# Optimization experiments

Measured on AMD Instinct MI355X. Metric: run time of the kernel, lower is better.

## Reference

```python
import jax, jax.numpy as jnp
import numpy as np

# Module config (init_kwargs)
K_PERIODS = 5
PMAX = 512
MIN_PERIOD_THRESHOLD = 2

B, T, N = 32, 2048, 128


def setup_inputs() -> dict:
    key = jax.random.key(0)
    x = jax.random.normal(key, (B, T, N), dtype=jnp.float32)
    return {"x": x}


def reference(x):
    """Faithful dense/padded JAX version of PeriodicityTransform.forward (mask=None).

    The torch module emits ragged PeriodGroups keyed by (cycles, period).
    Since jit requires static shapes, we return the same per-(series, freq)
    information in padded form:
      tiles   : [BN, K, T]  flattened folded tile (row-major cycle x period),
                 zero-padded past take = cycles*periods
      periods : [BN, K] int32
      cycles  : [BN, K] int32
    tiles[bn,k,:take].reshape(cycles, period) equals the torch tile exactly.
    """
    Bq, Tq, Nq = x.shape
    BN = Bq * Nq
    seqs = jnp.transpose(x, (0, 2, 1)).reshape(BN, Tq)  # [BN, T]

    # --- _topk_freq ---
    spec = jnp.fft.rfft(seqs, axis=-1)                   # [BN, T//2+1]
    mag2 = spec.real ** 2 + spec.imag ** 2
    mag2 = mag2.at[..., 0].set(0.0)                      # kill DC
    k = min(K_PERIODS, mag2.shape[-1] - 1)
    _, kidx = jax.lax.top_k(mag2, k)                     # [BN, K]
    kidx = jnp.maximum(kidx, 1).astype(jnp.int32)

    # --- period / cycle computation (valid_lengths == T, no mask) ---
    lengths = jnp.int32(Tq)
    periods = lengths // kidx                            # [BN, K]
    periods = jnp.minimum(periods, PMAX)
    min_period = min(MIN_PERIOD_THRESHOLD, Tq)
    periods = jnp.maximum(periods, min_period)
    periods = jnp.maximum(periods, 1)
    cycles = jnp.maximum(lengths // periods, 1)          # [BN, K]

    take = cycles * periods                              # [BN, K], <= T
    t = jnp.arange(Tq, dtype=jnp.int32)                  # [T]
    start = Tq - take                                    # [BN, K]
    gather_idx = jnp.clip(start[..., None] + t, 0, Tq - 1)  # [BN, K, T]
    valid = t[None, None, :] < take[..., None]           # [BN, K, T]

    src = jnp.broadcast_to(seqs[:, None, :], (BN, k, Tq))
    tiles = jnp.take_along_axis(src, gather_idx, axis=-1)
    tiles = jnp.where(valid, tiles, jnp.zeros((), dtype=tiles.dtype))
    return tiles, periods, cycles
```

## Files before the change

### kernel.cpp

```cpp
#include <hip/hip_runtime.h>

#define B_ 32
#define T_ 2048
#define N_ 128
#define K_ 5
#define BN_ (B_ * N_)
#define PMAX_ 512
#define MINP_ 2

static constexpr double PI_D = 3.14159265358979323846264338327950288;
static constexpr double S2_D = 0.70710678118654752440084436210485;

typedef float nfloat4 __attribute__((ext_vector_type(4)));

struct cd { double r, i; };

__device__ __forceinline__ void bf_w(cd& u, cd& v, double wr, double wi) {
    const double tr = v.r * wr - v.i * wi;
    const double ti = v.r * wi + v.i * wr;
    v.r = u.r - tr; v.i = u.i - ti;
    u.r += tr;      u.i += ti;
}
__device__ __forceinline__ void bf_1(cd& u, cd& v) {
    const double tr = v.r, ti = v.i;
    v.r = u.r - tr; v.i = u.i - ti;
    u.r += tr;      u.i += ti;
}
__device__ __forceinline__ void bf_mi(cd& u, cd& v) {
    const double tr = v.i, ti = -v.r;
    v.r = u.r - tr; v.i = u.i - ti;
    u.r += tr;      u.i += ti;
}
__device__ __forceinline__ int sw(int i) { return i ^ ((i >> 5) & 31); }

__global__ __launch_bounds__(256) void pt_twiddle(double2* __restrict__ tw) {
    const int m = blockIdx.x * 256 + threadIdx.x;
    if (m < 1024) {
        double s, c;
        sincos(-2.0 * PI_D * (double)m / 2048.0, &s, &c);
        tw[m] = make_double2(c, s);
    }
}

__global__ __launch_bounds__(256, 3) void pt_fft_tiles(const float* __restrict__ x,
                                                       float* __restrict__ out,
                                                       const double2* __restrict__ tw) {
    __shared__ double re[2048];
    __shared__ double im[2048];
    __shared__ __align__(16) float seqA[2052];
    __shared__ __align__(16) float seqB[2052];
    __shared__ double wredv[4];
    __shared__ int    wredi[4];
    __shared__ int sh_per[2][K_], sh_cyc[2][K_], sh_take[2][K_];

    const int i0  = blockIdx.x;
    const int q   = ((i0 & 7) << 8) | (i0 >> 3);
    const int bn0 = q * 2;
    const int b   = bn0 >> 7;
    const int n   = bn0 & 127;
    const int tid = threadIdx.x;

    const float* xp = x + (size_t)b * T_ * N_ + n;
#pragma unroll
    for (int m = 0; m < 8; ++m) {
        const int t = tid + 256 * m;
        const float2 v = *(const float2*)(xp + (size_t)t * N_);
        seqA[t] = v.x;
        seqB[t] = v.y;
        const int p = sw((int)(__brev((unsigned)t) >> 21));
        re[p] = (double)v.x;
        im[p] = (double)v.y;
    }
    __syncthreads();

    {
        const int base = tid * 8;
        cd E[8];
#pragma unroll
        for (int j = 0; j < 8; ++j) { const int p = sw(base + j); E[j].r = re[p]; E[j].i = im[p]; }
        bf_1(E[0], E[1]); bf_1(E[2], E[3]); bf_1(E[4], E[5]); bf_1(E[6], E[7]);
        bf_1(E[0], E[2]); bf_mi(E[1], E[3]); bf_1(E[4], E[6]); bf_mi(E[5], E[7]);
        bf_1(E[0], E[4]); bf_w(E[1], E[5], S2_D, -S2_D);
        bf_mi(E[2], E[6]); bf_w(E[3], E[7], -S2_D, -S2_D);
#pragma unroll
        for (int j = 0; j < 8; ++j) { const int p = sw(base + j); re[p] = E[j].r; im[p] = E[j].i; }
    }
    __syncthreads();

#pragma unroll
    for (int r = 0; r < 2; ++r) {
        const int s    = 4 + 3 * r;
        const int h    = 1 << (s - 1);
        const int bq   = tid & (h - 1);
        const int g    = tid >> (s - 1);
        const int base = g * 8 * h + bq;
        const double2 w1  = tw[bq << (11 - s)];
        const double2 w2a = tw[bq << (10 - s)];
        const double2 w2b = tw[(bq + h) << (10 - s)];
        const double2 w30 = tw[bq << (9 - s)];
        const double2 w31 = tw[(bq + h) << (9 - s)];
        const double2 w32 = tw[(bq + 2 * h) << (9 - s)];
        const double2 w33 = tw[(bq + 3 * h) << (9 - s)];
        cd E[8];
#pragma unroll
        for (int j = 0; j < 8; ++j) { const int p = sw(base + j * h); E[j].r = re[p]; E[j].i = im[p]; }
        bf_w(E[0], E[1], w1.x, w1.y);   bf_w(E[2], E[3], w1.x, w1.y);
        bf_w(E[4], E[5], w1.x, w1.y);   bf_w(E[6], E[7], w1.x, w1.y);
        bf_w(E[0], E[2], w2a.x, w2a.y); bf_w(E[1], E[3], w2b.x, w2b.y);
        bf_w(E[4], E[6], w2a.x, w2a.y); bf_w(E[5], E[7], w2b.x, w2b.y);
        bf_w(E[0], E[4], w30.x, w30.y); bf_w(E[1], E[5], w31.x, w31.y);
        bf_w(E[2], E[6], w32.x, w32.y); bf_w(E[3], E[7], w33.x, w33.y);
#pragma unroll
        for (int j = 0; j < 8; ++j) { const int p = sw(base + j * h); re[p] = E[j].r; im[p] = E[j].i; }
        __syncthreads();
    }

#pragma unroll
    for (int u = 0; u < 2; ++u) {
        const int bb = tid + 256 * u;
        const double2 wA = tw[bb << 1];
        const double2 wB = tw[bb];
        const double2 wC = tw[bb + 512];
        const int p0 = sw(bb), p1 = sw(bb + 512), p2 = sw(bb + 1024), p3 = sw(bb + 1536);
        cd E0 = {re[p0], im[p0]}, E1 = {re[p1], im[p1]};
        cd E2 = {re[p2], im[p2]}, E3 = {re[p3], im[p3]};
        bf_w(E0, E1, wA.x, wA.y); bf_w(E2, E3, wA.x, wA.y);
        bf_w(E0, E2, wB.x, wB.y); bf_w(E1, E3, wC.x, wC.y);
        re[p0] = E0.r; im[p0] = E0.i; re[p1] = E1.r; im[p1] = E1.i;
        re[p2] = E2.r; im[p2] = E2.i; re[p3] = E3.r; im[p3] = E3.i;
    }
    __syncthreads();

    double magsA[4], magsB[4];
#pragma unroll
    for (int m = 0; m < 4; ++m) {
        const int k  = 1 + tid + 256 * m;
        const int nk = 2048 - k;
        const int pk = sw(k), pn = sw(nk);
        const double zr = re[pk], zi = im[pk];
        const double yr = re[pn], yi = im[pn];
        const double ar = zr + yr, ai = zi - yi;
        const double br = zi + yi, bi = yr - zr;
        magsA[m] = ar * ar + ai * ai;
        magsB[m] = br * br + bi * bi;
    }
    __syncthreads();
#pragma unroll
    for (int m = 0; m < 4; ++m) {
        const int pk = sw(1 + tid + 256 * m);
        re[pk] = magsA[m];
        im[pk] = magsB[m];
    }
    __syncthreads();

    const int half = tid >> 7;
    const int lt   = tid & 127;
    const int wid  = tid >> 6;
    double* marr = half ? im : re;
    for (int it = 0; it < K_; ++it) {
        double bestv = -2.0;
        int    besti = 1 << 30;
#pragma unroll
        for (int m = 0; m < 8; ++m) {
            const int k = 1 + lt + 128 * m;
            const double v = marr[sw(k)];
            if (v > bestv || (v == bestv && k < besti)) { bestv = v; besti = k; }
        }
#pragma unroll
        for (int off = 32; off > 0; off >>= 1) {
            const double v2 = __shfl_down(bestv, off);
            const int    i2 = __shfl_down(besti, off);
            if (v2 > bestv || (v2 == bestv && i2 < besti)) { bestv = v2; besti = i2; }
        }
        if ((tid & 63) == 0) { wredv[wid] = bestv; wredi[wid] = besti; }
        __syncthreads();
        if (lt == 0) {
            double vb = wredv[2 * half]; int ib = wredi[2 * half];
            const double v1 = wredv[2 * half + 1]; const int i1 = wredi[2 * half + 1];
            if (v1 > vb || (v1 == vb && i1 < ib)) { vb = v1; ib = i1; }
            marr[sw(ib)] = -1.0;
            int period = T_ / ib;
            if (period > PMAX_) period = PMAX_;
            if (period < MINP_) period = MINP_;
            const int cyc = T_ / period;
            sh_per[half][it]  = period;
            sh_cyc[half][it]  = cyc;
            sh_take[half][it] = period * cyc;
        }
        __syncthreads();
    }

    const size_t TILES = (size_t)BN_ * K_ * T_;
    if (tid < 2 * K_) {
        const int s2 = tid / K_, k2 = tid % K_;
        out[TILES + (size_t)(bn0 + s2) * K_ + k2]                      = (float)sh_per[s2][k2];
        out[TILES + (size_t)BN_ * K_ + (size_t)(bn0 + s2) * K_ + k2]   = (float)sh_cyc[s2][k2];
    }

    float* rowA = out + (size_t)bn0 * (K_ * T_);
#pragma unroll
    for (int m = 0; m < 20; ++m) {
        const int e  = tid + 256 * m;
        const int s2 = (e >= K_ * (T_ / 4)) ? 1 : 0;
        const int w  = e - s2 * (K_ * (T_ / 4));
        const int k  = w >> 9;
        const int p4 = (w & 511) << 2;
        const int take  = sh_take[s2][k];
        const int start = T_ - take;
        const float4* sq4 = (const float4*)(s2 ? seqB : seqA);
        const int idx = start + p4;
        int a0 = idx >> 2;
        if (a0 > 511) a0 = 511;
        const int sh = idx & 3;
        const float4 lo = sq4[a0];
        const float4 hi = sq4[a0 + 1];
        float r0, r1, r2, r3;
        if (sh == 0)      { r0 = lo.x; r1 = lo.y; r2 = lo.z; r3 = lo.w; }
        else if (sh == 1) { r0 = lo.y; r1 = lo.z; r2 = lo.w; r3 = hi.x; }
        else if (sh == 2) { r0 = lo.z; r1 = lo.w; r2 = hi.x; r3 = hi.y; }
        else              { r0 = lo.w; r1 = hi.x; r2 = hi.y; r3 = hi.z; }
        nfloat4 v;
        v.x = (p4 + 0 < take) ? r0 : 0.0f;
        v.y = (p4 + 1 < take) ? r1 : 0.0f;
        v.z = (p4 + 2 < take) ? r2 : 0.0f;
        v.w = (p4 + 3 < take) ? r3 : 0.0f;
        __builtin_nontemporal_store(v, (nfloat4*)(rowA + (size_t)(s2 * K_ + k) * T_ + p4));
    }
}

extern "C" void kernel_launch(void* const* d_in, const int* in_sizes, int n_in,
                              void* d_out, int out_size, void* d_ws, size_t ws_size,
                              hipStream_t stream) {
    const float* x = (const float*)d_in[0];
    float* out = (float*)d_out;
    double2* tw = (double2*)d_ws;

    pt_twiddle<<<dim3(4), dim3(256), 0, stream>>>(tw);
    pt_fft_tiles<<<dim3(BN_ / 2), dim3(256), 0, stream>>>(x, out, tw);
}
```

Baseline: 245.2 us.

## Scatter tiles from register-held inputs instead of staging sequences in LDS

```diff
diff --git a/kernel.cpp b/kernel.cpp
--- a/kernel.cpp
+++ b/kernel.cpp
@@ -11,8 +11,6 @@
 static constexpr double PI_D = 3.14159265358979323846264338327950288;
 static constexpr double S2_D = 0.70710678118654752440084436210485;
 
-typedef float nfloat4 __attribute__((ext_vector_type(4)));
-
 struct cd { double r, i; };
 
 __device__ __forceinline__ void bf_w(cd& u, cd& v, double wr, double wi) {
@@ -42,16 +40,14 @@
     }
 }
 
-__global__ __launch_bounds__(256, 3) void pt_fft_tiles(const float* __restrict__ x,
+__global__ __launch_bounds__(256, 4) void pt_fft_tiles(const float* __restrict__ x,
                                                        float* __restrict__ out,
                                                        const double2* __restrict__ tw) {
     __shared__ double re[2048];
     __shared__ double im[2048];
-    __shared__ __align__(16) float seqA[2052];
-    __shared__ __align__(16) float seqB[2052];
     __shared__ double wredv[4];
     __shared__ int    wredi[4];
-    __shared__ int sh_per[2][K_], sh_cyc[2][K_], sh_take[2][K_];
+    __shared__ int sh_take[2][K_];
 
     const int i0  = blockIdx.x;
     const int q   = ((i0 & 7) << 8) | (i0 >> 3);
@@ -61,15 +57,17 @@
     const int tid = threadIdx.x;
 
     const float* xp = x + (size_t)b * T_ * N_ + n;
+    float2 v[8];
+#pragma unroll
+    for (int m = 0; m < 8; ++m)
+        v[m] = *(const float2*)(xp + (size_t)(tid + 256 * m) * N_);
+
 #pragma unroll
     for (int m = 0; m < 8; ++m) {
         const int t = tid + 256 * m;
-        const float2 v = *(const float2*)(xp + (size_t)t * N_);
-        seqA[t] = v.x;
-        seqB[t] = v.y;
         const int p = sw((int)(__brev((unsigned)t) >> 21));
-        re[p] = (double)v.x;
-        im[p] = (double)v.y;
+        re[p] = (double)v[m].x;
+        im[p] = (double)v[m].y;
     }
     __syncthreads();
 
@@ -163,8 +161,8 @@
 #pragma unroll
         for (int m = 0; m < 8; ++m) {
             const int k = 1 + lt + 128 * m;
-            const double v = marr[sw(k)];
-            if (v > bestv || (v == bestv && k < besti)) { bestv = v; besti = k; }
+            const double vv = marr[sw(k)];
+            if (vv > bestv || (vv == bestv && k < besti)) { bestv = vv; besti = k; }
         }
 #pragma unroll
         for (int off = 32; off > 0; off >>= 1) {
@@ -183,9 +181,7 @@
             if (period > PMAX_) period = PMAX_;
             if (period < MINP_) period = MINP_;
             const int cyc = T_ / period;
-            sh_per[half][it]  = period;
-            sh_cyc[half][it]  = cyc;
-            sh_take[half][it] = period * cyc;
+            sh_take[half][it] = (period << 16) | (period * cyc);
         }
         __syncthreads();
     }
@@ -193,38 +189,30 @@
     const size_t TILES = (size_t)BN_ * K_ * T_;
     if (tid < 2 * K_) {
         const int s2 = tid / K_, k2 = tid % K_;
-        out[TILES + (size_t)(bn0 + s2) * K_ + k2]                      = (float)sh_per[s2][k2];
-        out[TILES + (size_t)BN_ * K_ + (size_t)(bn0 + s2) * K_ + k2]   = (float)sh_cyc[s2][k2];
+        const int pk   = sh_take[s2][k2];
+        const int per  = pk >> 16;
+        const int take = pk & 0xFFFF;
+        out[TILES + (size_t)(bn0 + s2) * K_ + k2]                      = (float)per;
+        out[TILES + (size_t)BN_ * K_ + (size_t)(bn0 + s2) * K_ + k2]   = (float)(take / per);
     }
 
     float* rowA = out + (size_t)bn0 * (K_ * T_);
 #pragma unroll
-    for (int m = 0; m < 20; ++m) {
-        const int e  = tid + 256 * m;
-        const int s2 = (e >= K_ * (T_ / 4)) ? 1 : 0;
-        const int w  = e - s2 * (K_ * (T_ / 4));
-        const int k  = w >> 9;
-        const int p4 = (w & 511) << 2;
-        const int take  = sh_take[s2][k];
-        const int start = T_ - take;
-        const float4* sq4 = (const float4*)(s2 ? seqB : seqA);
-        const int idx = start + p4;
-        int a0 = idx >> 2;
-        if (a0 > 511) a0 = 511;
-        const int sh = idx & 3;
-        const float4 lo = sq4[a0];
-        const float4 hi = sq4[a0 + 1];
-        float r0, r1, r2, r3;
-        if (sh == 0)      { r0 = lo.x; r1 = lo.y; r2 = lo.z; r3 = lo.w; }
-        else if (sh == 1) { r0 = lo.y; r1 = lo.z; r2 = lo.w; r3 = hi.x; }
-        else if (sh == 2) { r0 = lo.z; r1 = lo.w; r2 = hi.x; r3 = hi.y; }
-        else              { r0 = lo.w; r1 = hi.x; r2 = hi.y; r3 = hi.z; }
-        nfloat4 v;
-        v.x = (p4 + 0 < take) ? r0 : 0.0f;
-        v.y = (p4 + 1 < take) ? r1 : 0.0f;
-        v.z = (p4 + 2 < take) ? r2 : 0.0f;
-        v.w = (p4 + 3 < take) ? r3 : 0.0f;
-        __builtin_nontemporal_store(v, (nfloat4*)(rowA + (size_t)(s2 * K_ + k) * T_ + p4));
+    for (int s2 = 0; s2 < 2; ++s2) {
+#pragma unroll
+        for (int k = 0; k < K_; ++k) {
+            const int take  = sh_take[s2][k] & 0xFFFF;
+            const int start = T_ - take;
+            float* dst = rowA + (size_t)(s2 * K_ + k) * T_;
+#pragma unroll
+            for (int m = 0; m < 8; ++m) {
+                const int t   = tid + 256 * m;
+                const bool lo = (t < start);
+                const int p   = lo ? (t + take) : (t - start);
+                const float val = lo ? 0.0f : (s2 ? v[m].y : v[m].x);
+                __builtin_nontemporal_store(val, dst + p);
+            }
+        }
     }
 }
 
```

After: 232.4 us. 1.06x faster.
